# Optimization experiments

Hardware: AMD Instinct MI355X
Metric: run time of the kernel (lower is better)

## Reference

```python
import jax, jax.numpy as jnp
import numpy as np

B, C, N, H = 4, 256, 1024, 8
D = C // H
EPS = 1e-5

def setup_inputs() -> dict:
    key = jax.random.key(0)
    ks = jax.random.split(key, 10)
    s = lambda k, shape: (jax.random.normal(k, shape, jnp.float32) * 0.02)
    return dict(
        node_embeds=jax.random.normal(ks[0], (B, C, N), jnp.float32),
        edge_embeds=jax.random.normal(ks[1], (B, N, N), jnp.float32),
        da_prior=jax.random.normal(ks[2], (B, N, C), jnp.float32),
        gamma=jnp.ones((C,), jnp.float32),
        beta=jnp.zeros((C,), jnp.float32),
        w_qkv=s(ks[3], (C, 3 * C)),            # Linear(node_dim, 3*node_dim), no bias
        w_proj=s(ks[4], (C, C)),
        b_proj=jnp.zeros((C,), jnp.float32),
        w_expand=s(ks[5], (H,)),               # Conv2d(1,H,1) weight (per-head scalar)
        b_expand=jnp.zeros((H,), jnp.float32),
        w_reduce=s(ks[6], (H,)),               # Conv2d(H,1,1) weight
        b_reduce=jnp.zeros((1,), jnp.float32),
        w_fc=s(ks[7], (1, C)),                 # Linear(edge_dim=1, node_dim)
        b_fc=jnp.zeros((C,), jnp.float32),
    )

def reference(node_embeds, edge_embeds, da_prior, gamma, beta, w_qkv,
              w_proj, b_proj, w_expand, b_expand, w_reduce, b_reduce, w_fc, b_fc):
    x = jnp.swapaxes(node_embeds, 1, 2)                       # [B,N,C]
    # einsum 'bnn,bnc->bnc': diagonal of edge matrix scales each node
    diag = jnp.diagonal(edge_embeds, axis1=1, axis2=2)        # [B,N]
    attned = diag[:, :, None] * x                             # [B,N,C]
    # einsum 'bnc,bca->bnc' with prior permuted [B,C,A]: multiply by sum over A
    prior_sum = da_prior.sum(axis=1)                          # [B,C]
    x = attned * prior_sum[:, None, :] + x                    # residual add
    # LayerNorm over channel dim
    mu = x.mean(-1, keepdims=True)
    var = x.var(-1, keepdims=True)
    ln = (x - mu) * jax.lax.rsqrt(var + EPS) * gamma + beta
    qkv = (ln @ w_qkv).reshape(B, N, 3, H, D)
    q = jnp.transpose(qkv[:, :, 0], (0, 2, 1, 3))             # [B,H,N,D]
    k = jnp.transpose(qkv[:, :, 1], (0, 2, 1, 3))
    v = jnp.transpose(qkv[:, :, 2], (0, 2, 1, 3))
    scale = D ** -0.5
    attn = jnp.einsum('bhnd,bhmd->bhnm', q, k) * scale        # [B,H,N,N]
    bias = edge_embeds[:, None] * w_expand[None, :, None, None] + b_expand[None, :, None, None]
    attn = attn + bias                                        # pre-softmax scores = residual
    a = jax.nn.softmax(attn, axis=-1)
    node = jnp.einsum('bhnm,bhmd->bnhd', a, v).reshape(B, N, C)
    # reduce conv over heads on (softmax + residual)
    edge = jnp.einsum('bhnm,h->bnm', a + attn, w_reduce) + b_reduce[0]  # [B,N,N]
    w = jax.nn.softmax(edge, axis=-1)
    wsum = (w * edge).sum(-1)                                 # [B,N]
    node = node + wsum[:, :, None] @ w_fc + b_fc              # fc: [B,N,1]@[1,C]
    node = node @ w_proj + b_proj
    return jnp.swapaxes(node, 1, 2), edge                     # ([B,C,N], [B,N,N])
```

## Files before the change

### kernel.cpp

```cpp
#include <hip/hip_runtime.h>
#include <math.h>

#define Bn 4
#define Cn 256
#define Nn 1024
#define Hn 8
#define Dn 32
#define BHND (Bn * Hn * Nn * Dn)
#define BHN  (Bn * Hn * Nn)

typedef short bf16x8 __attribute__((ext_vector_type(8)));
typedef float f32x4 __attribute__((ext_vector_type(4)));

__device__ inline unsigned f2bf_rn_bits(float x) {
  union { float f; unsigned u; } v; v.f = x;
  return (v.u + 0x7FFFu + ((v.u >> 16) & 1u)) >> 16;
}
__device__ inline float bfbits2f(unsigned b) {
  union { unsigned u; float f; } v; v.u = b << 16; return v.f;
}
__device__ inline void split_bf(float x, unsigned& hi, unsigned& lo) {
  hi = f2bf_rn_bits(x);
  lo = f2bf_rn_bits(x - bfbits2f(hi));
}
__device__ inline unsigned split_bf_trunc_pack(float x) {
  union { float f; unsigned u; } v; v.f = x;
  unsigned hi = v.u >> 16;
  union { unsigned u; float f; } hv; hv.u = hi << 16;
  union { float f; unsigned u; } r; r.f = x - hv.f;
  return hi | (r.u & 0xffff0000u);
}
__device__ inline void unpack_u32x8(const uint4& a, const uint4& b, bf16x8& hi, bf16x8& lo) {
  int4 h4, l4;
  h4.x = (int)((a.x & 0xffffu) | (a.y << 16));  l4.x = (int)((a.x >> 16) | (a.y & 0xffff0000u));
  h4.y = (int)((a.z & 0xffffu) | (a.w << 16));  l4.y = (int)((a.z >> 16) | (a.w & 0xffff0000u));
  h4.z = (int)((b.x & 0xffffu) | (b.y << 16));  l4.z = (int)((b.x >> 16) | (b.y & 0xffff0000u));
  h4.w = (int)((b.z & 0xffffu) | (b.w << 16));  l4.w = (int)((b.z >> 16) | (b.w & 0xffff0000u));
  hi = *(bf16x8*)&h4; lo = *(bf16x8*)&l4;
}

__global__ __launch_bounds__(256) void k_pre(const float* __restrict__ w,
                                             const float* __restrict__ dap,
                                             short* __restrict__ wt_h,
                                             short* __restrict__ wt_l,
                                             float* __restrict__ pp) {
  __shared__ float tile[32][33];
  int bi = blockIdx.x;
  if (bi < 32) {
    int b = bi >> 3, ch = bi & 7;
    int c = threadIdx.x;
    float s = 0.f;
    int n0 = ch * 128;
    for (int n = n0; n < n0 + 128; ++n) s += dap[(size_t)(b * Nn + n) * Cn + c];
    pp[(size_t)bi * Cn + c] = s;
  } else {
    int wi = bi - 32;
    int j0 = (wi >> 3) << 5;
    int k0 = (wi & 7) << 5;
    int tx = threadIdx.x & 31, ty = threadIdx.x >> 5;
#pragma unroll
    for (int i = 0; i < 4; ++i)
      tile[ty + i * 8][tx] = w[(size_t)(k0 + ty + i * 8) * 768 + j0 + tx];
    __syncthreads();
#pragma unroll
    for (int i = 0; i < 4; ++i) {
      float v = tile[tx][ty + i * 8];
      unsigned hb, lb; split_bf(v, hb, lb);
      wt_h[(size_t)(j0 + ty + i * 8) * 256 + k0 + tx] = (short)hb;
      wt_l[(size_t)(j0 + ty + i * 8) * 256 + k0 + tx] = (short)lb;
    }
  }
}

__global__ __launch_bounds__(256) void k_prep_ln(const float* __restrict__ ne,
                                                 const float* __restrict__ eg,
                                                 const float* __restrict__ pp,
                                                 const float* __restrict__ gamma,
                                                 const float* __restrict__ beta,
                                                 short* __restrict__ ln_h,
                                                 short* __restrict__ ln_l) {
  int bn = blockIdx.x;
  int b = bn >> 10, n = bn & 1023;
  int c = threadIdx.x;
  float x = ne[(size_t)(b * Cn + c) * Nn + n];
  float pr = 0.f;
#pragma unroll
  for (int ch = 0; ch < 8; ++ch) pr += pp[(size_t)(b * 8 + ch) * Cn + c];
  float dg = eg[(size_t)(b * Nn + n) * Nn + n];
  float x2 = x * (1.f + dg * pr);
  float s = x2, qq = x2 * x2;
#pragma unroll
  for (int off = 32; off >= 1; off >>= 1) {
    s += __shfl_xor(s, off);
    qq += __shfl_xor(qq, off);
  }
  __shared__ float ss[4], sq[4];
  if ((c & 63) == 0) { ss[c >> 6] = s; sq[c >> 6] = qq; }
  __syncthreads();
  s = ss[0] + ss[1] + ss[2] + ss[3];
  qq = sq[0] + sq[1] + sq[2] + sq[3];
  float mu = s * (1.f / 256.f);
  float var = qq * (1.f / 256.f) - mu * mu;
  float r = rsqrtf(var + 1e-5f);
  float v = (x2 - mu) * r * gamma[c] + beta[c];
  unsigned hb, lb; split_bf(v, hb, lb);
  ln_h[(size_t)bn * Cn + c] = (short)hb;
  ln_l[(size_t)bn * Cn + c] = (short)lb;
}

__global__ __launch_bounds__(256) void k_qkv_mfma(
    const short* __restrict__ ln_h, const short* __restrict__ ln_l,
    const short* __restrict__ wt_h, const short* __restrict__ wt_l,
    short* __restrict__ q_hi, short* __restrict__ q_lo,
    short* __restrict__ k_hi, short* __restrict__ k_lo,
    short* __restrict__ vt_hi, short* __restrict__ vt_lo) {
  __shared__ short Ah[64 * 40];
  __shared__ short Al[64 * 40];
  __shared__ short Bh[64 * 40];
  __shared__ short Bl[64 * 40];
  __shared__ float ct[64][65];
  int m0 = blockIdx.x * 64;
  int j0 = blockIdx.y * 64;
  int t = threadIdx.x, wid = t >> 6, l = t & 63;
  int lr = l & 15, lq = l >> 4;
  f32x4 acc[4] = {};
  int row = t >> 2, ch = (t & 3) * 8;
  const short* a_h_src = ln_h + (size_t)(m0 + row) * 256 + ch;
  const short* a_l_src = ln_l + (size_t)(m0 + row) * 256 + ch;
  const short* b_h_src = wt_h + (size_t)(j0 + row) * 256 + ch;
  const short* b_l_src = wt_l + (size_t)(j0 + row) * 256 + ch;
  uint4 vah = *(const uint4*)&a_h_src[0];
  uint4 val = *(const uint4*)&a_l_src[0];
  uint4 vbh = *(const uint4*)&b_h_src[0];
  uint4 vbl = *(const uint4*)&b_l_src[0];
  for (int it = 0; it < 8; ++it) {
    __syncthreads();
    *(uint4*)&Ah[row * 40 + ch] = vah;
    *(uint4*)&Al[row * 40 + ch] = val;
    *(uint4*)&Bh[row * 40 + ch] = vbh;
    *(uint4*)&Bl[row * 40 + ch] = vbl;
    __syncthreads();
    int kn = ((it + 1) & 7) * 32;
    vah = *(const uint4*)&a_h_src[kn];
    val = *(const uint4*)&a_l_src[kn];
    vbh = *(const uint4*)&b_h_src[kn];
    vbl = *(const uint4*)&b_l_src[kn];
    bf16x8 ah = *(bf16x8*)&Ah[(wid * 16 + lr) * 40 + lq * 8];
    bf16x8 al8 = *(bf16x8*)&Al[(wid * 16 + lr) * 40 + lq * 8];
#pragma unroll
    for (int js = 0; js < 4; ++js) {
      bf16x8 bh = *(bf16x8*)&Bh[(js * 16 + lr) * 40 + lq * 8];
      bf16x8 bl = *(bf16x8*)&Bl[(js * 16 + lr) * 40 + lq * 8];
      acc[js] = __builtin_amdgcn_mfma_f32_16x16x32_bf16(al8, bh, acc[js], 0, 0, 0);
      acc[js] = __builtin_amdgcn_mfma_f32_16x16x32_bf16(ah, bl, acc[js], 0, 0, 0);
      acc[js] = __builtin_amdgcn_mfma_f32_16x16x32_bf16(ah, bh, acc[js], 0, 0, 0);
    }
  }
  __syncthreads();
#pragma unroll
  for (int js = 0; js < 4; ++js)
#pragma unroll
    for (int reg = 0; reg < 4; ++reg)
      ct[wid * 16 + lq * 4 + reg][js * 16 + lr] = acc[js][reg];
  __syncthreads();
  int b = m0 >> 10, n0 = m0 & 1023;
  int three = j0 >> 8;
  const float scale = 0.17677669529663687f;
  if (three == 2) {
    int jl = t >> 2;
    int n4 = (t & 3) * 16;
    int rem = (j0 & 255) + jl;
    int h = rem >> 5, d = rem & 31;
    short hs[16], ls[16];
#pragma unroll
    for (int u = 0; u < 16; ++u) {
      unsigned hb, lb;
      split_bf(ct[n4 + u][jl], hb, lb);
      hs[u] = (short)hb; ls[u] = (short)lb;
    }
    size_t ob = ((size_t)(b * Hn + h) * Dn + d) * Nn + n0 + n4;
    *(uint4*)&vt_hi[ob] = *(uint4*)&hs[0];
    *(uint4*)&vt_hi[ob + 8] = *(uint4*)&hs[8];
    *(uint4*)&vt_lo[ob] = *(uint4*)&ls[0];
    *(uint4*)&vt_lo[ob + 8] = *(uint4*)&ls[8];
  } else {
    int m_l = t & 63, half = t >> 6;
    int rem = (j0 & 255) + half * 16;
    int h = rem >> 5, ddb = rem & 31;
    int n = n0 + m_l;
    float sc = (three == 0) ? 1.0f : scale;
    short* dh = three ? k_hi : q_hi;
    short* dl = three ? k_lo : q_lo;
    short hs[16], ls[16];
#pragma unroll
    for (int u = 0; u < 16; ++u) {
      unsigned hb, lb;
      split_bf(ct[m_l][half * 16 + u] * sc, hb, lb);
      hs[u] = (short)hb; ls[u] = (short)lb;
    }
    size_t base = ((size_t)((b * Hn + h) * Nn + n)) * Dn + ddb;
    *(uint4*)&dh[base] = *(uint4*)&hs[0];
    *(uint4*)&dh[base + 8] = *(uint4*)&hs[8];
    *(uint4*)&dl[base] = *(uint4*)&ls[0];
    *(uint4*)&dl[base + 8] = *(uint4*)&ls[8];
  }
}

__global__ __launch_bounds__(256, 4) void k_attn_core(
    const short* __restrict__ q_hi, const short* __restrict__ q_lo,
    const short* __restrict__ k_hi, const short* __restrict__ k_lo,
    const short* __restrict__ vt_hi, const short* __restrict__ vt_lo,
    const float* __restrict__ eg,
    const float* __restrict__ w_expand, const float* __restrict__ b_expand,
    float* __restrict__ o_part, float* __restrict__ l_part) {
  __shared__ short kh[64 * 40];
  __shared__ short kl[64 * 40];
  __shared__ short vth[32 * 72];
  __shared__ short vtl[32 * 72];
  __shared__ unsigned pbuf[4][16 * 68];

  int blk = blockIdx.x;
  int mh = blk & 1;
  int nt = (blk >> 1) & 15;
  int h = (blk >> 5) & 7;
  int b = blk >> 8;
  int n0 = nt * 64;
  int t = threadIdx.x, wid = t >> 6, l = t & 63;
  int lr = l & 15, lq = l >> 4;

  const float we = w_expand[h], be = b_expand[h];
  size_t bhb = (size_t)(b * Hn + h) * Nn * Dn;
  const short* khg = k_hi + bhb;
  const short* klg = k_lo + bhb;
  const short* vhg = vt_hi + bhb;
  const short* vlg = vt_lo + bhb;

  bf16x8 qhi, qlo;
  {
    size_t qoff = bhb + (size_t)(n0 + wid * 16 + lr) * Dn + lq * 8;
    qhi = *(const bf16x8*)&q_hi[qoff];
    qlo = *(const bf16x8*)&q_lo[qoff];
  }

  int srow = t >> 2, sc = (t & 3) * 8;
  int sd = t >> 3, scm = (t & 7) * 8;
  uint4 rkh, rkl, rvh, rvl;
  {
    int m0 = mh * 512;
    rkh = *(const uint4*)&khg[(size_t)(m0 + srow) * Dn + sc];
    rkl = *(const uint4*)&klg[(size_t)(m0 + srow) * Dn + sc];
    rvh = *(const uint4*)&vhg[(size_t)sd * Nn + m0 + scm];
    rvl = *(const uint4*)&vlg[(size_t)sd * Nn + m0 + scm];
  }

  f32x4 O0 = {0.f, 0.f, 0.f, 0.f}, O1 = {0.f, 0.f, 0.f, 0.f};
  float rowsum[4] = {0.f, 0.f, 0.f, 0.f};
  int nrow = n0 + wid * 16 + lq * 4;

  for (int ms = 0; ms < 8; ++ms) {
    int m0 = mh * 512 + ms * 64;
    float eb[4][4];
#pragma unroll
    for (int reg = 0; reg < 4; ++reg) {
      const float* ep = &eg[(size_t)(b * Nn + nrow + reg) * Nn + m0 + lr];
#pragma unroll
      for (int msub = 0; msub < 4; ++msub) eb[msub][reg] = ep[msub * 16];
    }
    __syncthreads();
    *(uint4*)&kh[srow * 40 + sc] = rkh;
    *(uint4*)&kl[srow * 40 + sc] = rkl;
    *(uint4*)&vth[sd * 72 + scm] = rvh;
    *(uint4*)&vtl[sd * 72 + scm] = rvl;
    __syncthreads();
    {
      int mn0 = mh * 512 + ((ms < 7) ? ms + 1 : ms) * 64;
      rkh = *(const uint4*)&khg[(size_t)(mn0 + srow) * Dn + sc];
      rkl = *(const uint4*)&klg[(size_t)(mn0 + srow) * Dn + sc];
      rvh = *(const uint4*)&vhg[(size_t)sd * Nn + mn0 + scm];
      rvl = *(const uint4*)&vlg[(size_t)sd * Nn + mn0 + scm];
    }

#pragma unroll
    for (int msub = 0; msub < 4; ++msub) {
      int mrow = msub * 16 + lr;
      bf16x8 bh8 = *(bf16x8*)&kh[mrow * 40 + lq * 8];
      bf16x8 bl8 = *(bf16x8*)&kl[mrow * 40 + lq * 8];
      f32x4 sacc = {0.f, 0.f, 0.f, 0.f};
      sacc = __builtin_amdgcn_mfma_f32_16x16x32_bf16(qlo, bh8, sacc, 0, 0, 0);
      sacc = __builtin_amdgcn_mfma_f32_16x16x32_bf16(qhi, bl8, sacc, 0, 0, 0);
      sacc = __builtin_amdgcn_mfma_f32_16x16x32_bf16(qhi, bh8, sacc, 0, 0, 0);
#pragma unroll
      for (int reg = 0; reg < 4; ++reg) {
        float s = sacc[reg] + eb[msub][reg] * we + be;
        float e = __expf(s);
        rowsum[reg] += e;
        pbuf[wid][(lq * 4 + reg) * 68 + msub * 16 + lr] = split_bf_trunc_pack(e);
      }
    }

#pragma unroll
    for (int mw = 0; mw < 2; ++mw) {
      uint4 pa = *(uint4*)&pbuf[wid][lr * 68 + mw * 32 + lq * 8];
      uint4 pb = *(uint4*)&pbuf[wid][lr * 68 + mw * 32 + lq * 8 + 4];
      bf16x8 ahi, alo;
      unpack_u32x8(pa, pb, ahi, alo);
      {
        bf16x8 vh8 = *(bf16x8*)&vth[lr * 72 + mw * 32 + lq * 8];
        bf16x8 vl8 = *(bf16x8*)&vtl[lr * 72 + mw * 32 + lq * 8];
        O0 = __builtin_amdgcn_mfma_f32_16x16x32_bf16(alo, vh8, O0, 0, 0, 0);
        O0 = __builtin_amdgcn_mfma_f32_16x16x32_bf16(ahi, vl8, O0, 0, 0, 0);
        O0 = __builtin_amdgcn_mfma_f32_16x16x32_bf16(ahi, vh8, O0, 0, 0, 0);
      }
      {
        bf16x8 vh8 = *(bf16x8*)&vth[(16 + lr) * 72 + mw * 32 + lq * 8];
        bf16x8 vl8 = *(bf16x8*)&vtl[(16 + lr) * 72 + mw * 32 + lq * 8];
        O1 = __builtin_amdgcn_mfma_f32_16x16x32_bf16(alo, vh8, O1, 0, 0, 0);
        O1 = __builtin_amdgcn_mfma_f32_16x16x32_bf16(ahi, vl8, O1, 0, 0, 0);
        O1 = __builtin_amdgcn_mfma_f32_16x16x32_bf16(ahi, vh8, O1, 0, 0, 0);
      }
    }
  }

#pragma unroll
  for (int reg = 0; reg < 4; ++reg) {
#pragma unroll
    for (int off = 1; off < 16; off <<= 1)
      rowsum[reg] += __shfl_xor(rowsum[reg], off);
  }
  size_t pbase = (size_t)mh * BHND + bhb;
#pragma unroll
  for (int reg = 0; reg < 4; ++reg) {
    int n = nrow + reg;
    o_part[pbase + (size_t)n * Dn + lr] = O0[reg];
    o_part[pbase + (size_t)n * Dn + 16 + lr] = O1[reg];
    if (lr == 0)
      l_part[(size_t)mh * BHN + (size_t)(b * Hn + h) * Nn + n] = rowsum[reg];
  }
}

__global__ __launch_bounds__(256, 4) void k_edge_mfma(
    const short* __restrict__ q_hi, const short* __restrict__ q_lo,
    const short* __restrict__ k_hi, const short* __restrict__ k_lo,
    const float* __restrict__ eg, const float* __restrict__ l_part,
    const float* __restrict__ w_expand, const float* __restrict__ b_expand,
    const float* __restrict__ w_reduce, const float* __restrict__ b_reduce,
    float* __restrict__ edge_out, float* __restrict__ pl_part,
    float* __restrict__ pwe_part) {
  __shared__ short kh[64 * 40];
  __shared__ short kl[64 * 40];
  int blk = blockIdx.x;
  int mt = blk & 15;
  int nt = (blk >> 4) & 15;
  int b = blk >> 8;
  int n0 = nt * 64, m0 = mt * 64;
  int t = threadIdx.x, wid = t >> 6, l = t & 63;
  int lr = l & 15, lq = l >> 4;
  const float br = b_reduce[0];
  int nrow = n0 + wid * 16 + lq * 4;

  float eacc[4][4], ebias[4][4];
#pragma unroll
  for (int reg = 0; reg < 4; ++reg) {
    const float* ep = &eg[(size_t)(b * Nn + nrow + reg) * Nn + m0 + lr];
#pragma unroll
    for (int msub = 0; msub < 4; ++msub) {
      ebias[msub][reg] = ep[msub * 16];
      eacc[msub][reg] = br;
    }
  }

  int srow = t >> 2, sc = (t & 3) * 8;
  uint4 rkh, rkl;
  {
    size_t bhb0 = (size_t)(b * Hn) * Nn * Dn;
    rkh = *(const uint4*)&k_hi[bhb0 + (size_t)(m0 + srow) * Dn + sc];
    rkl = *(const uint4*)&k_lo[bhb0 + (size_t)(m0 + srow) * Dn + sc];
  }

  for (int h = 0; h < Hn; ++h) {
    size_t bhb = (size_t)(b * Hn + h) * Nn * Dn;
    float we = w_expand[h], be = b_expand[h], wr = w_reduce[h];
    bf16x8 qhi, qlo;
    {
      size_t qoff = bhb + (size_t)(n0 + wid * 16 + lr) * Dn + lq * 8;
      qhi = *(const bf16x8*)&q_hi[qoff];
      qlo = *(const bf16x8*)&q_lo[qoff];
    }
    float invl[4];
#pragma unroll
    for (int reg = 0; reg < 4; ++reg) {
      size_t idx = (size_t)(b * Hn + h) * Nn + nrow + reg;
      invl[reg] = 1.0f / (l_part[idx] + l_part[BHN + idx]);
    }

    __syncthreads();
    *(uint4*)&kh[srow * 40 + sc] = rkh;
    *(uint4*)&kl[srow * 40 + sc] = rkl;
    __syncthreads();
    {
      size_t bhn = (size_t)(b * Hn + ((h < 7) ? h + 1 : h)) * Nn * Dn;
      rkh = *(const uint4*)&k_hi[bhn + (size_t)(m0 + srow) * Dn + sc];
      rkl = *(const uint4*)&k_lo[bhn + (size_t)(m0 + srow) * Dn + sc];
    }
#pragma unroll
    for (int msub = 0; msub < 4; ++msub) {
      int mrow = msub * 16 + lr;
      bf16x8 bh8 = *(bf16x8*)&kh[mrow * 40 + lq * 8];
      bf16x8 bl8 = *(bf16x8*)&kl[mrow * 40 + lq * 8];
      f32x4 sacc = {0.f, 0.f, 0.f, 0.f};
      sacc = __builtin_amdgcn_mfma_f32_16x16x32_bf16(qlo, bh8, sacc, 0, 0, 0);
      sacc = __builtin_amdgcn_mfma_f32_16x16x32_bf16(qhi, bl8, sacc, 0, 0, 0);
      sacc = __builtin_amdgcn_mfma_f32_16x16x32_bf16(qhi, bh8, sacc, 0, 0, 0);
#pragma unroll
      for (int reg = 0; reg < 4; ++reg) {
        float s = sacc[reg] + ebias[msub][reg] * we + be;
        float p = __expf(s) * invl[reg];
        eacc[msub][reg] += wr * (p + s);
      }
    }
  }
#pragma unroll
  for (int msub = 0; msub < 4; ++msub)
#pragma unroll
    for (int reg = 0; reg < 4; ++reg)
      edge_out[(size_t)(b * Nn + nrow + reg) * Nn + m0 + msub * 16 + lr] = eacc[msub][reg];

  float pl[4] = {0.f, 0.f, 0.f, 0.f}, pw[4] = {0.f, 0.f, 0.f, 0.f};
#pragma unroll
  for (int msub = 0; msub < 4; ++msub)
#pragma unroll
    for (int reg = 0; reg < 4; ++reg) {
      float e = eacc[msub][reg];
      float x = __expf(e);
      pl[reg] += x;
      pw[reg] += x * e;
    }
#pragma unroll
  for (int reg = 0; reg < 4; ++reg) {
#pragma unroll
    for (int off = 1; off < 16; off <<= 1) {
      pl[reg] += __shfl_xor(pl[reg], off);
      pw[reg] += __shfl_xor(pw[reg], off);
    }
    if (lr == 0) {
      int idx = mt * (Bn * Nn) + b * Nn + nrow + reg;
      pl_part[idx] = pl[reg];
      pwe_part[idx] = pw[reg];
    }
  }
}

__global__ __launch_bounds__(256) void k_proj_gemm(const float* __restrict__ o_part,
                                                   const float* __restrict__ l_part,
                                                   const float* __restrict__ pl,
                                                   const float* __restrict__ pwe,
                                                   const float* __restrict__ wfc,
                                                   const float* __restrict__ bfc,
                                                   const float* __restrict__ wproj,
                                                   const float* __restrict__ bproj,
                                                   float* __restrict__ out) {
  __shared__ __align__(16) float at[16][68];
  __shared__ __align__(16) float bt[16][68];
  __shared__ float ct[64][65];
  __shared__ float wsm_s[64];
  int m0 = blockIdx.x * 64;
  int j0 = blockIdx.y * 64;
  int t = threadIdx.x;
  int tx = t & 15, ty = t >> 4;
  if (t < 64) {
    int m = m0 + t;
    float L = 0.f, Wv = 0.f;
#pragma unroll
    for (int mt = 0; mt < 16; ++mt) {
      L += pl[mt * (Bn * Nn) + m];
      Wv += pwe[mt * (Bn * Nn) + m];
    }
    wsm_s[t] = Wv / L;
  }
  __syncthreads();
  float4 acc[4] = {};
  for (int k0 = 0; k0 < 256; k0 += 16) {
    {
      int row = t >> 2, k4 = (t & 3) << 2;
      int m = m0 + row;
      int bb = m >> 10, n = m & 1023;
      int c = k0 + k4;
      int h = c >> 5, dd = c & 31;
      float wsm = wsm_s[row];
      size_t ob = ((size_t)(bb * Hn + h) * Nn + n) * Dn + dd;
      float4 oa = *(const float4*)&o_part[ob];
      float4 oc = *(const float4*)&o_part[BHND + ob];
      size_t sidx = (size_t)(bb * Hn + h) * Nn + n;
      float inv = 1.0f / (l_part[sidx] + l_part[BHN + sidx]);
      float4 a;
      a.x = (oa.x + oc.x) * inv + wsm * wfc[c + 0] + bfc[c + 0];
      a.y = (oa.y + oc.y) * inv + wsm * wfc[c + 1] + bfc[c + 1];
      a.z = (oa.z + oc.z) * inv + wsm * wfc[c + 2] + bfc[c + 2];
      a.w = (oa.w + oc.w) * inv + wsm * wfc[c + 3] + bfc[c + 3];
      at[k4 + 0][row] = a.x; at[k4 + 1][row] = a.y;
      at[k4 + 2][row] = a.z; at[k4 + 3][row] = a.w;
      int rb = t >> 4, jb = (t & 15) << 2;
      *(float4*)&bt[rb][jb] = *(const float4*)&wproj[(size_t)(k0 + rb) * 256 + j0 + jb];
    }
    __syncthreads();
#pragma unroll
    for (int kk = 0; kk < 16; ++kk) {
      float4 a4 = *(float4*)&at[kk][ty << 2];
      float4 b4 = *(float4*)&bt[kk][tx << 2];
      acc[0].x += a4.x * b4.x; acc[0].y += a4.x * b4.y; acc[0].z += a4.x * b4.z; acc[0].w += a4.x * b4.w;
      acc[1].x += a4.y * b4.x; acc[1].y += a4.y * b4.y; acc[1].z += a4.y * b4.z; acc[1].w += a4.y * b4.w;
      acc[2].x += a4.z * b4.x; acc[2].y += a4.z * b4.y; acc[2].z += a4.z * b4.z; acc[2].w += a4.z * b4.w;
      acc[3].x += a4.w * b4.x; acc[3].y += a4.w * b4.y; acc[3].z += a4.w * b4.z; acc[3].w += a4.w * b4.w;
    }
    __syncthreads();
  }
#pragma unroll
  for (int i = 0; i < 4; ++i) {
    ct[(ty << 2) + i][(tx << 2) + 0] = acc[i].x + bproj[j0 + (tx << 2) + 0];
    ct[(ty << 2) + i][(tx << 2) + 1] = acc[i].y + bproj[j0 + (tx << 2) + 1];
    ct[(ty << 2) + i][(tx << 2) + 2] = acc[i].z + bproj[j0 + (tx << 2) + 2];
    ct[(ty << 2) + i][(tx << 2) + 3] = acc[i].w + bproj[j0 + (tx << 2) + 3];
  }
  __syncthreads();
  int b = m0 >> 10, n0 = m0 & 1023;
  int n4 = t & 15, c0i = t >> 4;
#pragma unroll
  for (int u = 0; u < 4; ++u) {
    int ci = c0i + u * 16;
    float4 val = { ct[(n4 << 2) + 0][ci], ct[(n4 << 2) + 1][ci],
                   ct[(n4 << 2) + 2][ci], ct[(n4 << 2) + 3][ci] };
    *(float4*)&out[(size_t)(b * Cn + j0 + ci) * Nn + n0 + (n4 << 2)] = val;
  }
}

extern "C" void kernel_launch(void* const* d_in, const int* in_sizes, int n_in,
                              void* d_out, int out_size, void* d_ws, size_t ws_size,
                              hipStream_t stream) {
  (void)in_sizes; (void)n_in; (void)out_size; (void)ws_size;
  const float* node_embeds = (const float*)d_in[0];
  const float* edge_embeds = (const float*)d_in[1];
  const float* da_prior    = (const float*)d_in[2];
  const float* gamma       = (const float*)d_in[3];
  const float* beta        = (const float*)d_in[4];
  const float* w_qkv       = (const float*)d_in[5];
  const float* w_proj      = (const float*)d_in[6];
  const float* b_proj      = (const float*)d_in[7];
  const float* w_expand    = (const float*)d_in[8];
  const float* b_expand    = (const float*)d_in[9];
  const float* w_reduce    = (const float*)d_in[10];
  const float* b_reduce    = (const float*)d_in[11];
  const float* w_fc        = (const float*)d_in[12];
  const float* b_fc        = (const float*)d_in[13];
  float* out_node = (float*)d_out;
  float* out_edge = out_node + (size_t)Bn * Cn * Nn;

  const size_t M = 1048576;
  float* W = (float*)d_ws;
  short* ln_hi  = (short*)(W + M);
  short* ln_lo  = ln_hi + M;
  float* o_part = W;
  short* vt_hi  = (short*)(W + 2 * M);
  short* vt_lo  = vt_hi + M;
  short* q_hi   = (short*)(W + 3 * M);
  short* q_lo   = q_hi + M;
  short* k_hi   = q_hi + 2 * M;
  short* k_lo   = q_hi + 3 * M;
  float* ws_pp    = W + 5 * M;
  float* l_part   = ws_pp + Bn * 8 * Cn;
  float* pl_part  = l_part + 2 * BHN;
  float* pwe_part = pl_part + 16 * Bn * Nn;
  short* wt_hi    = (short*)(pwe_part + 16 * Bn * Nn);
  short* wt_lo    = wt_hi + 768 * 256;

  k_pre<<<dim3(224), dim3(256), 0, stream>>>(w_qkv, da_prior, wt_hi, wt_lo, ws_pp);
  k_prep_ln<<<dim3(Bn * Nn), dim3(256), 0, stream>>>(node_embeds, edge_embeds, ws_pp,
                                                     gamma, beta, ln_hi, ln_lo);
  k_qkv_mfma<<<dim3(64, 12), dim3(256), 0, stream>>>(ln_hi, ln_lo, wt_hi, wt_lo,
                                                     q_hi, q_lo, k_hi, k_lo,
                                                     vt_hi, vt_lo);
  k_attn_core<<<dim3(Bn * Hn * 16 * 2), dim3(256), 0, stream>>>(
      q_hi, q_lo, k_hi, k_lo, vt_hi, vt_lo, edge_embeds, w_expand, b_expand,
      o_part, l_part);
  k_edge_mfma<<<dim3(Bn * 16 * 16), dim3(256), 0, stream>>>(
      q_hi, q_lo, k_hi, k_lo, edge_embeds, l_part, w_expand, b_expand,
      w_reduce, b_reduce, out_edge, pl_part, pwe_part);
  k_proj_gemm<<<dim3(64, 4), dim3(256), 0, stream>>>(o_part, l_part, pl_part,
                                                     pwe_part, w_fc, b_fc,
                                                     w_proj, b_proj, out_node);
}
```

Baseline: 185.6 us.

## Move projection GEMM to split-bf16 MFMA and raise wave priority in attention loops

The scalar FP32 output-projection GEMM is replaced by a split-bf16 (hi/lo) MFMA GEMM. The prep kernel gains extra blocks that transpose w_proj and split it into bf16 hi/lo halves. Separately, s_setprio hints are wrapped around the MFMA/exp sections of the attention and edge kernels so those waves get issue priority over waves doing loads. The three-MFMA split keeps near-FP32 accuracy, but adds conversion work and extra barriers per K-step.

After: 174.8 us. 5.8% less time.

```diff
diff --git a/kernel.cpp b/kernel.cpp
--- a/kernel.cpp
+++ b/kernel.cpp
@@ -40,9 +40,12 @@
 }
 
 __global__ __launch_bounds__(256) void k_pre(const float* __restrict__ w,
+                                             const float* __restrict__ wp,
                                              const float* __restrict__ dap,
                                              short* __restrict__ wt_h,
                                              short* __restrict__ wt_l,
+                                             short* __restrict__ wpt_h,
+                                             short* __restrict__ wpt_l,
                                              float* __restrict__ pp) {
   __shared__ float tile[32][33];
   int bi = blockIdx.x;
@@ -53,7 +56,7 @@
     int n0 = ch * 128;
     for (int n = n0; n < n0 + 128; ++n) s += dap[(size_t)(b * Nn + n) * Cn + c];
     pp[(size_t)bi * Cn + c] = s;
-  } else {
+  } else if (bi < 224) {
     int wi = bi - 32;
     int j0 = (wi >> 3) << 5;
     int k0 = (wi & 7) << 5;
@@ -68,6 +71,22 @@
       unsigned hb, lb; split_bf(v, hb, lb);
       wt_h[(size_t)(j0 + ty + i * 8) * 256 + k0 + tx] = (short)hb;
       wt_l[(size_t)(j0 + ty + i * 8) * 256 + k0 + tx] = (short)lb;
+    }
+  } else {
+    int wi = bi - 224;
+    int j0 = (wi >> 3) << 5;
+    int k0 = (wi & 7) << 5;
+    int tx = threadIdx.x & 31, ty = threadIdx.x >> 5;
+#pragma unroll
+    for (int i = 0; i < 4; ++i)
+      tile[ty + i * 8][tx] = wp[(size_t)(k0 + ty + i * 8) * 256 + j0 + tx];
+    __syncthreads();
+#pragma unroll
+    for (int i = 0; i < 4; ++i) {
+      float v = tile[tx][ty + i * 8];
+      unsigned hb, lb; split_bf(v, hb, lb);
+      wpt_h[(size_t)(j0 + ty + i * 8) * 256 + k0 + tx] = (short)hb;
+      wpt_l[(size_t)(j0 + ty + i * 8) * 256 + k0 + tx] = (short)lb;
     }
   }
 }
@@ -280,6 +299,7 @@
       rvl = *(const uint4*)&vlg[(size_t)sd * Nn + mn0 + scm];
     }
 
+    __builtin_amdgcn_s_setprio(1);
 #pragma unroll
     for (int msub = 0; msub < 4; ++msub) {
       int mrow = msub * 16 + lr;
@@ -297,7 +317,9 @@
         pbuf[wid][(lq * 4 + reg) * 68 + msub * 16 + lr] = split_bf_trunc_pack(e);
       }
     }
-
+    __builtin_amdgcn_s_setprio(0);
+
+    __builtin_amdgcn_s_setprio(1);
 #pragma unroll
     for (int mw = 0; mw < 2; ++mw) {
       uint4 pa = *(uint4*)&pbuf[wid][lr * 68 + mw * 32 + lq * 8];
@@ -319,6 +341,7 @@
         O1 = __builtin_amdgcn_mfma_f32_16x16x32_bf16(ahi, vh8, O1, 0, 0, 0);
       }
     }
+    __builtin_amdgcn_s_setprio(0);
   }
 
 #pragma unroll
@@ -402,6 +425,7 @@
       rkh = *(const uint4*)&k_hi[bhn + (size_t)(m0 + srow) * Dn + sc];
       rkl = *(const uint4*)&k_lo[bhn + (size_t)(m0 + srow) * Dn + sc];
     }
+    __builtin_amdgcn_s_setprio(1);
 #pragma unroll
     for (int msub = 0; msub < 4; ++msub) {
       int mrow = msub * 16 + lr;
@@ -418,6 +442,7 @@
         eacc[msub][reg] += wr * (p + s);
       }
     }
+    __builtin_amdgcn_s_setprio(0);
   }
 #pragma unroll
   for (int msub = 0; msub < 4; ++msub)
@@ -450,23 +475,22 @@
   }
 }
 
-__global__ __launch_bounds__(256) void k_proj_gemm(const float* __restrict__ o_part,
-                                                   const float* __restrict__ l_part,
-                                                   const float* __restrict__ pl,
-                                                   const float* __restrict__ pwe,
-                                                   const float* __restrict__ wfc,
-                                                   const float* __restrict__ bfc,
-                                                   const float* __restrict__ wproj,
-                                                   const float* __restrict__ bproj,
-                                                   float* __restrict__ out) {
-  __shared__ __align__(16) float at[16][68];
-  __shared__ __align__(16) float bt[16][68];
+__global__ __launch_bounds__(256) void k_proj_mfma(
+    const float* __restrict__ o_part, const float* __restrict__ l_part,
+    const float* __restrict__ pl, const float* __restrict__ pwe,
+    const float* __restrict__ wfc, const float* __restrict__ bfc,
+    const short* __restrict__ wpt_h, const short* __restrict__ wpt_l,
+    const float* __restrict__ bproj, float* __restrict__ out) {
+  __shared__ short Ah[64 * 40];
+  __shared__ short Al[64 * 40];
+  __shared__ short Bh[64 * 40];
+  __shared__ short Bl[64 * 40];
   __shared__ float ct[64][65];
   __shared__ float wsm_s[64];
   int m0 = blockIdx.x * 64;
   int j0 = blockIdx.y * 64;
-  int t = threadIdx.x;
-  int tx = t & 15, ty = t >> 4;
+  int t = threadIdx.x, wid = t >> 6, l = t & 63;
+  int lr = l & 15, lq = l >> 4;
   if (t < 64) {
     int m = m0 + t;
     float L = 0.f, Wv = 0.f;
@@ -478,49 +502,56 @@
     wsm_s[t] = Wv / L;
   }
   __syncthreads();
-  float4 acc[4] = {};
-  for (int k0 = 0; k0 < 256; k0 += 16) {
-    {
-      int row = t >> 2, k4 = (t & 3) << 2;
-      int m = m0 + row;
-      int bb = m >> 10, n = m & 1023;
-      int c = k0 + k4;
-      int h = c >> 5, dd = c & 31;
-      float wsm = wsm_s[row];
-      size_t ob = ((size_t)(bb * Hn + h) * Nn + n) * Dn + dd;
-      float4 oa = *(const float4*)&o_part[ob];
-      float4 oc = *(const float4*)&o_part[BHND + ob];
-      size_t sidx = (size_t)(bb * Hn + h) * Nn + n;
-      float inv = 1.0f / (l_part[sidx] + l_part[BHN + sidx]);
-      float4 a;
-      a.x = (oa.x + oc.x) * inv + wsm * wfc[c + 0] + bfc[c + 0];
-      a.y = (oa.y + oc.y) * inv + wsm * wfc[c + 1] + bfc[c + 1];
-      a.z = (oa.z + oc.z) * inv + wsm * wfc[c + 2] + bfc[c + 2];
-      a.w = (oa.w + oc.w) * inv + wsm * wfc[c + 3] + bfc[c + 3];
-      at[k4 + 0][row] = a.x; at[k4 + 1][row] = a.y;
-      at[k4 + 2][row] = a.z; at[k4 + 3][row] = a.w;
-      int rb = t >> 4, jb = (t & 15) << 2;
-      *(float4*)&bt[rb][jb] = *(const float4*)&wproj[(size_t)(k0 + rb) * 256 + j0 + jb];
-    }
-    __syncthreads();
-#pragma unroll
-    for (int kk = 0; kk < 16; ++kk) {
-      float4 a4 = *(float4*)&at[kk][ty << 2];
-      float4 b4 = *(float4*)&bt[kk][tx << 2];
-      acc[0].x += a4.x * b4.x; acc[0].y += a4.x * b4.y; acc[0].z += a4.x * b4.z; acc[0].w += a4.x * b4.w;
-      acc[1].x += a4.y * b4.x; acc[1].y += a4.y * b4.y; acc[1].z += a4.y * b4.z; acc[1].w += a4.y * b4.w;
-      acc[2].x += a4.z * b4.x; acc[2].y += a4.z * b4.y; acc[2].z += a4.z * b4.z; acc[2].w += a4.z * b4.w;
-      acc[3].x += a4.w * b4.x; acc[3].y += a4.w * b4.y; acc[3].z += a4.w * b4.z; acc[3].w += a4.w * b4.w;
-    }
-    __syncthreads();
-  }
-#pragma unroll
-  for (int i = 0; i < 4; ++i) {
-    ct[(ty << 2) + i][(tx << 2) + 0] = acc[i].x + bproj[j0 + (tx << 2) + 0];
-    ct[(ty << 2) + i][(tx << 2) + 1] = acc[i].y + bproj[j0 + (tx << 2) + 1];
-    ct[(ty << 2) + i][(tx << 2) + 2] = acc[i].z + bproj[j0 + (tx << 2) + 2];
-    ct[(ty << 2) + i][(tx << 2) + 3] = acc[i].w + bproj[j0 + (tx << 2) + 3];
-  }
+  f32x4 acc[4] = {};
+  int row = t >> 2, kc = (t & 3) * 8;
+  int m = m0 + row;
+  int bb = m >> 10, n = m & 1023;
+  for (int it = 0; it < 8; ++it) {
+    int c = it * 32 + kc;
+    int h = c >> 5;
+    size_t sidx = (size_t)(bb * Hn + h) * Nn + n;
+    float inv = 1.0f / (l_part[sidx] + l_part[BHN + sidx]);
+    float wsm = wsm_s[row];
+    size_t ob = ((size_t)(bb * Hn + h) * Nn + n) * Dn + (c & 31);
+    float4 oa0 = *(const float4*)&o_part[ob];
+    float4 oa1 = *(const float4*)&o_part[ob + 4];
+    float4 oc0 = *(const float4*)&o_part[BHND + ob];
+    float4 oc1 = *(const float4*)&o_part[BHND + ob + 4];
+    float av[8];
+    av[0] = (oa0.x + oc0.x) * inv; av[1] = (oa0.y + oc0.y) * inv;
+    av[2] = (oa0.z + oc0.z) * inv; av[3] = (oa0.w + oc0.w) * inv;
+    av[4] = (oa1.x + oc1.x) * inv; av[5] = (oa1.y + oc1.y) * inv;
+    av[6] = (oa1.z + oc1.z) * inv; av[7] = (oa1.w + oc1.w) * inv;
+    short hs[8], ls[8];
+#pragma unroll
+    for (int j = 0; j < 8; ++j) {
+      float a = av[j] + wsm * wfc[c + j] + bfc[c + j];
+      unsigned hb, lb; split_bf(a, hb, lb);
+      hs[j] = (short)hb; ls[j] = (short)lb;
+    }
+    __syncthreads();
+    *(uint4*)&Ah[row * 40 + kc] = *(uint4*)&hs[0];
+    *(uint4*)&Al[row * 40 + kc] = *(uint4*)&ls[0];
+    *(uint4*)&Bh[row * 40 + kc] = *(const uint4*)&wpt_h[(size_t)(j0 + row) * 256 + c];
+    *(uint4*)&Bl[row * 40 + kc] = *(const uint4*)&wpt_l[(size_t)(j0 + row) * 256 + c];
+    __syncthreads();
+    bf16x8 ah = *(bf16x8*)&Ah[(wid * 16 + lr) * 40 + lq * 8];
+    bf16x8 al8 = *(bf16x8*)&Al[(wid * 16 + lr) * 40 + lq * 8];
+#pragma unroll
+    for (int js = 0; js < 4; ++js) {
+      bf16x8 bh = *(bf16x8*)&Bh[(js * 16 + lr) * 40 + lq * 8];
+      bf16x8 bl = *(bf16x8*)&Bl[(js * 16 + lr) * 40 + lq * 8];
+      acc[js] = __builtin_amdgcn_mfma_f32_16x16x32_bf16(al8, bh, acc[js], 0, 0, 0);
+      acc[js] = __builtin_amdgcn_mfma_f32_16x16x32_bf16(ah, bl, acc[js], 0, 0, 0);
+      acc[js] = __builtin_amdgcn_mfma_f32_16x16x32_bf16(ah, bh, acc[js], 0, 0, 0);
+    }
+  }
+  __syncthreads();
+#pragma unroll
+  for (int js = 0; js < 4; ++js)
+#pragma unroll
+    for (int reg = 0; reg < 4; ++reg)
+      ct[wid * 16 + lq * 4 + reg][js * 16 + lr] = acc[js][reg] + bproj[j0 + js * 16 + lr];
   __syncthreads();
   int b = m0 >> 10, n0 = m0 & 1023;
   int n4 = t & 15, c0i = t >> 4;
@@ -571,8 +602,11 @@
   float* pwe_part = pl_part + 16 * Bn * Nn;
   short* wt_hi    = (short*)(pwe_part + 16 * Bn * Nn);
   short* wt_lo    = wt_hi + 768 * 256;
-
-  k_pre<<<dim3(224), dim3(256), 0, stream>>>(w_qkv, da_prior, wt_hi, wt_lo, ws_pp);
+  short* wpt_hi   = wt_lo + 768 * 256;
+  short* wpt_lo   = wpt_hi + 256 * 256;
+
+  k_pre<<<dim3(288), dim3(256), 0, stream>>>(w_qkv, w_proj, da_prior,
+                                             wt_hi, wt_lo, wpt_hi, wpt_lo, ws_pp);
   k_prep_ln<<<dim3(Bn * Nn), dim3(256), 0, stream>>>(node_embeds, edge_embeds, ws_pp,
                                                      gamma, beta, ln_hi, ln_lo);
   k_qkv_mfma<<<dim3(64, 12), dim3(256), 0, stream>>>(ln_hi, ln_lo, wt_hi, wt_lo,
@@ -584,7 +618,8 @@
   k_edge_mfma<<<dim3(Bn * 16 * 16), dim3(256), 0, stream>>>(
       q_hi, q_lo, k_hi, k_lo, edge_embeds, l_part, w_expand, b_expand,
       w_reduce, b_reduce, out_edge, pl_part, pwe_part);
-  k_proj_gemm<<<dim3(64, 4), dim3(256), 0, stream>>>(o_part, l_part, pl_part,
+  k_proj_mfma<<<dim3(64, 4), dim3(256), 0, stream>>>(o_part, l_part, pl_part,
                                                      pwe_part, w_fc, b_fc,
-                                                     w_proj, b_proj, out_node);
-}
+                                                     wpt_hi, wpt_lo, b_proj,
+                                                     out_node);
+}
```
